# Kernel tuning notes

Measured on AMD Instinct MI355X. Metric: run time of the kernel, lower is better.

The kernel has to match this reference:

```python
import jax, jax.numpy as jnp
import numpy as np
from jax import lax

N, T, E = 20000, 64, 640000
H, OUT, HEADS = 128, 64, 3
NEG_SLOPE = 0.2  # GATConv default negative_slope


def setup_inputs() -> dict:
    key = jax.random.key(0)
    ks = jax.random.split(key, 10)
    s = 0.1
    return {
        "node_features": jax.random.normal(ks[0], (N, T), jnp.float32),
        "edge_index": jax.random.randint(ks[1], (2, E), 0, N, dtype=jnp.int32),
        "edge_attributes": jax.random.uniform(ks[2], (E,), jnp.float32),
        "lstm_Wih": jax.random.normal(ks[3], (4 * H, 1), jnp.float32) * s,
        "lstm_Whh": jax.random.normal(ks[4], (4 * H, H), jnp.float32) * s,
        "lstm_bih": jnp.zeros((4 * H,), jnp.float32),
        "lstm_bhh": jnp.zeros((4 * H,), jnp.float32),
        "gcn_W": jax.random.normal(ks[5], (H, H), jnp.float32) * s,
        "gcn_b": jnp.zeros((H,), jnp.float32),
        "gat_W": jax.random.normal(ks[6], (HEADS * OUT, H), jnp.float32) * s,
        "gat_att_src": jax.random.normal(ks[7], (HEADS, OUT), jnp.float32) * s,
        "gat_att_dst": jax.random.normal(ks[8], (HEADS, OUT), jnp.float32) * s,
        "gat_b": jnp.zeros((HEADS * OUT,), jnp.float32),
    }


def _lstm_last(x, Wih, Whh, bih, bhh):
    """x: [N, T, 1] -> last hidden state [N, H] (torch gate order i,f,g,o)."""
    n = x.shape[0]
    h_dim = Whh.shape[1]
    b = bih + bhh

    def step(carry, xt):
        h, c = carry
        g = xt @ Wih.T + h @ Whh.T + b  # [N, 4H]
        i, f, gg, o = jnp.split(g, 4, axis=-1)
        c = jax.nn.sigmoid(f) * c + jax.nn.sigmoid(i) * jnp.tanh(gg)
        h = jax.nn.sigmoid(o) * jnp.tanh(c)
        return (h, c), None

    init = (jnp.zeros((n, h_dim), x.dtype), jnp.zeros((n, h_dim), x.dtype))
    (h, _), _ = lax.scan(step, init, jnp.swapaxes(x, 0, 1))
    return h


def _add_self_loops(row, col, n):
    loop = jnp.arange(n, dtype=row.dtype)
    return jnp.concatenate([row, loop]), jnp.concatenate([col, loop])


def _gcn(x, row, col, edge_weight, W, b):
    """PyG GCNConv: self-loops (weight 1), symmetric normalization, W x + b."""
    n = x.shape[0]
    row, col = _add_self_loops(row, col, n)
    ew = jnp.concatenate([edge_weight, jnp.ones((n,), edge_weight.dtype)])
    x = x @ W.T  # [N, H]
    deg = jax.ops.segment_sum(ew, col, num_segments=n)
    dinv = jnp.where(deg > 0, deg ** -0.5, 0.0)
    norm = dinv[row] * ew * dinv[col]  # [E+N]
    out = jax.ops.segment_sum(x[row] * norm[:, None], col, num_segments=n)
    return out + b


def _gat(x, row, col, W, att_src, att_dst, b):
    """PyG GATConv (concat=True): self-loops, edge softmax over incoming edges."""
    n = x.shape[0]
    heads, c = att_src.shape
    xh = (x @ W.T).reshape(n, heads, c)  # [N, Hd, C]
    a_src = jnp.einsum('nhc,hc->nh', xh, att_src)  # [N, Hd]
    a_dst = jnp.einsum('nhc,hc->nh', xh, att_dst)
    row, col = _add_self_loops(row, col, n)
    alpha = jax.nn.leaky_relu(a_src[row] + a_dst[col], NEG_SLOPE)  # [E', Hd]
    amax = jax.ops.segment_max(alpha, col, num_segments=n)
    alpha = jnp.exp(alpha - amax[col])
    denom = jax.ops.segment_sum(alpha, col, num_segments=n)
    alpha = alpha / denom[col]
    out = jax.ops.segment_sum(xh[row] * alpha[:, :, None], col, num_segments=n)
    return out.reshape(n, heads * c) + b


def reference(node_features, edge_index, edge_attributes,
              lstm_Wih, lstm_Whh, lstm_bih, lstm_bhh,
              gcn_W, gcn_b, gat_W, gat_att_src, gat_att_dst, gat_b):
    x = node_features[:, :, None]  # [N, T, 1]
    x = _lstm_last(x, lstm_Wih, lstm_Whh, lstm_bih, lstm_bhh)  # [N, H]
    x = jax.nn.relu(x)
    row, col = edge_index[0], edge_index[1]
    x = _gcn(x, row, col, edge_attributes, gcn_W, gcn_b)
    x = jax.nn.relu(x)
    x = _gat(x, row, col, gat_W, gat_att_src, gat_att_dst, gat_b)  # [N, Hd*C]
    return jnp.mean(x, axis=0, keepdims=True)  # global_mean_pool, batch=None -> [1, Hd*C]
```

## Files before the change

kernel.cpp:

```cpp
#include <hip/hip_runtime.h>


#define N_NODES 20000
#define T_STEPS 64
#define N_EDGES 640000
#define HDIM    128
#define JOUT    192
#define NEG_SLOPE 0.2f
#define EDGE_CAP 128
#define NBW     16
#define NGRP    5
#define NBB     (NBW * NGRP)
#define BTHR    640
#define LDS_W     131072
#define LDS_BW    4096
#define LDS_SCR   (NGRP * 4096)
#define LDS_FLG   256
#define LDS_TOTAL (LDS_W + LDS_BW + LDS_SCR + LDS_FLG)

#define L2E  1.4426950408889634f
#define K2E  2.8853900817779268f

typedef _Float16 half8 __attribute__((ext_vector_type(8)));
typedef _Float16 half4v __attribute__((ext_vector_type(4)));
typedef _Float16 half2v __attribute__((ext_vector_type(2)));
typedef float floatx4 __attribute__((ext_vector_type(4)));

__device__ __forceinline__ float lrelu(float x) { return x > 0.f ? x : NEG_SLOPE * x; }

__global__ void pack_whh_kernel(const float* __restrict__ Whh,
                                _Float16* __restrict__ Wpack)
{
  int i = blockIdx.x * 256 + threadIdx.x;
  int tile = i >> 6, lane = i & 63;
  int nt = tile >> 2, kt = tile & 3;
  int row = nt * 16 + (lane & 15);
  int c0  = kt * 32 + (lane >> 4) * 8;
  const float sc = ((row >> 7) == 2) ? K2E : L2E;
  half8 v;
  #pragma unroll
  for (int j = 0; j < 8; ++j)
    v[j] = (_Float16)(Whh[row * 128 + c0 + j] * sc);
  *(half8*)&Wpack[(size_t)i * 8] = v;
}

template <int M>
__global__ void pack_w_kernel(const float* __restrict__ W,
                              _Float16* __restrict__ P)
{
  int i = blockIdx.x * 256 + threadIdx.x;
  int tile = i >> 6, lane = i & 63;
  int mt = tile >> 2, kt = tile & 3;
  int row = mt * 16 + (lane & 15);
  int c0  = kt * 32 + (lane >> 4) * 8;
  half8 v;
  #pragma unroll
  for (int j = 0; j < 8; ++j)
    v[j] = (_Float16)W[row * 128 + c0 + j];
  *(half8*)&P[(size_t)i * 8] = v;
}


#define INITACC(L, acc) do {                                                  \
  _Pragma("unroll") for (int g_ = 0; g_ < 4; ++g_) {                          \
    const float4 p0_ = *(const float4*)&bwRole[g_ * 128 + (L) * 16];          \
    const float4 p1_ = *(const float4*)&bwRole[g_ * 128 + (L) * 16 + 2];      \
    acc[g_][0] = p0_.x + xv * p0_.y;                                          \
    acc[g_][1] = p0_.z + xv * p0_.w;                                          \
    acc[g_][2] = p1_.x + xv * p1_.y;                                          \
    acc[g_][3] = p1_.z + xv * p1_.w;                                          \
  }                                                                           \
} while (0)

#define LDA(buf, L, KT) do {                                                  \
  _Pragma("unroll") for (int g_ = 0; g_ < 4; ++g_)                            \
    buf[g_] = *(const half8*)&WlRole[g_ * 16384 + (L) * 2048 + (KT) * 512];   \
} while (0)

#define MFA(acc, buf, KT) do {                                                \
  _Pragma("unroll") for (int g_ = 0; g_ < 4; ++g_)                            \
    acc[g_] = __builtin_amdgcn_mfma_f32_16x16x32_f16(                         \
        buf[g_], Bf[(KT)], acc[g_], 0, 0, 0);                                 \
} while (0)

#define PHASE4(L, acc) do {                                                   \
  const int cg_ = cgb + (L);                                                  \
  half4v hpack;                                                               \
  _Pragma("unroll") for (int r_ = 0; r_ < 4; ++r_) {                          \
    const float Be = __builtin_amdgcn_exp2f(-acc[0][r_]);                     \
    const float Ae = __builtin_amdgcn_exp2f(-acc[1][r_]);                     \
    const float De = __builtin_amdgcn_exp2f(acc[2][r_]);                      \
    const float Ee = __builtin_amdgcn_exp2f(-acc[3][r_]);                     \
    const float Ap = Ae + 1.f;                                                \
    const float Bp = Be + 1.f;                                                \
    const float Dp = De + 1.f;                                                \
    const float Nn = cst[(L) * 4 + r_] * Bp * Dp + Ap * (De - 1.f);           \
    const float cv = Nn * __builtin_amdgcn_rcpf(Ap * Bp * Dp);                \
    cst[(L) * 4 + r_] = cv;                                                   \
    const float cvc = fminf(fmaxf(cv, -10.f), 10.f);                          \
    const float Fe = __builtin_amdgcn_exp2f(K2E * cvc);                       \
    hpack[r_] = (_Float16)((Fe - 1.f) *                                       \
                __builtin_amdgcn_rcpf((Ee + 1.f) * (Fe + 1.f)));              \
  }                                                                           \
  const int lp_ = nl + 16 * (2 * (cg_ & 1) + wq_hi);                          \
  *(half4v*)&myscr[(cg_ >> 1) * 512 + lp_ * 8 + j0] = hpack;                  \
} while (0)

#define SB __builtin_amdgcn_sched_barrier(0)

#define SIGNAL(arr, val) do {                                                 \
  __threadfence_block();                                                      \
  if (ln == 0) arr[wv] = (val);                                               \
} while (0)
#define WAITGE(arr, val) do {                                                 \
  if (ln == 0) { while (arr[pw] < (val)) __builtin_amdgcn_s_sleep(1); }       \
  __builtin_amdgcn_wave_barrier();                                            \
  __threadfence_block();                                                      \
} while (0)

#define LSTM_STEP(t) do {                                                     \
  WAITGE(flW, (t));                                                           \
  half8 Bf[4];                                                                \
  _Pragma("unroll") for (int kt_ = 0; kt_ < 4; ++kt_)                         \
    Bf[kt_] = *(const half8*)&scrLane[kt_ * 512];                             \
  SIGNAL(flR, (t) + 1);                                                       \
  floatx4 accA[4], accB[4];                                                   \
  half8 Aa[4], Ab[4];                                                         \
                                                                  \
  INITACC(0, accA);                                                           \
  LDA(Aa, 0, 0); LDA(Ab, 0, 1);                                               \
  MFA(accA, Aa, 0); LDA(Aa, 0, 2);                                            \
  MFA(accA, Ab, 1); LDA(Ab, 0, 3);                                            \
  MFA(accA, Aa, 2); MFA(accA, Ab, 3);                                         \
                                                                  \
  INITACC(1, accB); LDA(Aa, 1, 0); LDA(Ab, 1, 1);                             \
  WAITGE(flR, (t) + 1);                                                       \
  SB; PHASE4(0, accA);                                                        \
  MFA(accB, Aa, 0); LDA(Aa, 1, 2);                                            \
  MFA(accB, Ab, 1); LDA(Ab, 1, 3);                                            \
  MFA(accB, Aa, 2); MFA(accB, Ab, 3);                                         \
                                                                  \
  INITACC(2, accA); LDA(Aa, 2, 0); LDA(Ab, 2, 1);                             \
  SB; PHASE4(1, accB);                                                        \
  MFA(accA, Aa, 0); LDA(Aa, 2, 2);                                            \
  MFA(accA, Ab, 1); LDA(Ab, 2, 3);                                            \
  MFA(accA, Aa, 2); MFA(accA, Ab, 3);                                         \
                                                                  \
  INITACC(3, accB); LDA(Aa, 3, 0); LDA(Ab, 3, 1);                             \
  SB; PHASE4(2, accA);                                                        \
  MFA(accB, Aa, 0); LDA(Aa, 3, 2);                                            \
  MFA(accB, Ab, 1); LDA(Ab, 3, 3);                                            \
  MFA(accB, Aa, 2); MFA(accB, Ab, 3);                                         \
  PHASE4(3, accB);                                                            \
  SIGNAL(flW, (t) + 1);                                                       \
} while (0)

__global__ __attribute__((amdgpu_flat_work_group_size(BTHR, BTHR),
                          amdgpu_waves_per_eu(3, 3)))
void lstm_stream_kernel(
    const float* __restrict__ xfeat, const _Float16* __restrict__ Wpack,
    const float* __restrict__ Wih, const float* __restrict__ bih,
    const float* __restrict__ bhh, _Float16* __restrict__ x1)
{
  extern __shared__ char dynlds[];
  _Float16* Wl  = (_Float16*)dynlds;
  float2*   bw  = (float2*)(dynlds + LDS_W);
  _Float16* scr = (_Float16*)(dynlds + LDS_W + LDS_BW);
  volatile int* flR = (volatile int*)(dynlds + LDS_W + LDS_BW + LDS_SCR);
  volatile int* flW = flR + 16;

  const int tid  = threadIdx.x;
  const int wv   = tid >> 6;
  const int pw   = wv ^ 1;
  const int grp  = wv >> 1;
  const int role = wv & 1;
  const int cgb  = role * 4;
  const int ln   = tid & 63;
  const int nl   = ln & 15;
  const int quad = ln >> 4;
  const int n0   = blockIdx.x * NBB + grp * NBW;

  {
    const float4* src = (const float4*)Wpack;
    float4* dst = (float4*)Wl;
    for (int i = tid; i < LDS_W / 16; i += BTHR) dst[i] = src[i];
  }
  for (int i = tid; i < 512; i += BTHR) {
    const float sc = ((i >> 7) == 2) ? K2E : L2E;
    bw[i] = make_float2((bih[i] + bhh[i]) * sc, Wih[i] * sc);
  }
  {
    float4* z = (float4*)scr;
    for (int i = tid; i < LDS_SCR / 16; i += BTHR)
      z[i] = make_float4(0.f, 0.f, 0.f, 0.f);
  }
  if (tid < 32) { flR[tid] = 0; flW[tid] = 0; }
  __syncthreads();

  _Float16* myscr = scr + grp * 2048;
  const _Float16* WlRole  = Wl + (size_t)cgb * 2048 + (size_t)ln * 8;
  const float2*   bwRole  = bw + cgb * 16 + quad * 4;
  const _Float16* scrLane = myscr + (size_t)ln * 8;
  const float* xrow = xfeat + (size_t)(n0 + nl) * T_STEPS;

  float cst[16];
  #pragma unroll
  for (int i = 0; i < 16; ++i) cst[i] = 0.f;

  const int wq_hi = quad >> 1;
  const int j0    = (quad & 1) * 4;

  float xv = xrow[0];

  #pragma unroll 1
  for (int t = 0; t < T_STEPS; ++t) {
    const float xn = xrow[(t + 1 <= 63) ? (t + 1) : 63];
    LSTM_STEP(t);
    xv = xn;
  }

  #pragma unroll
  for (int k = 0; k < 2; ++k) {
    const int kt = role * 2 + k;
    half8 hf = *(const half8*)&scrLane[kt * 512];
    #pragma unroll
    for (int j = 0; j < 8; ++j)
      hf[j] = (_Float16)fmaxf((float)hf[j], 0.f);
    *(half8*)&x1[(size_t)(n0 + nl) * HDIM + kt * 32 + quad * 8] = hf;
  }
}

template <int J>
__global__ __launch_bounds__(320) void gemm_mfma(
    const _Float16* __restrict__ X, const _Float16* __restrict__ P,
    _Float16* __restrict__ Y)
{
  const int ln = threadIdx.x & 63;
  const int wv = threadIdx.x >> 6;
  const int node = blockIdx.x * 80 + wv * 16 + (ln & 15);
  const int ko = (ln >> 4) * 8;
  half8 Bf[4];
  #pragma unroll
  for (int kt = 0; kt < 4; ++kt)
    Bf[kt] = *(const half8*)&X[(size_t)node * 128 + kt * 32 + ko];
  #pragma unroll
  for (int m = 0; m < J / 16; ++m) {
    floatx4 acc = {0.f, 0.f, 0.f, 0.f};
    #pragma unroll
    for (int kt = 0; kt < 4; ++kt) {
      const half8 Af = *(const half8*)&P[(size_t)((m * 4 + kt) * 64 + ln) * 8];
      acc = __builtin_amdgcn_mfma_f32_16x16x32_f16(Af, Bf[kt], acc, 0, 0, 0);
    }
    half4v o;
    #pragma unroll
    for (int j = 0; j < 4; ++j) o[j] = (_Float16)acc[j];
    *(half4v*)&Y[(size_t)node * J + m * 16 + (ln >> 4) * 4] = o;
  }
}

__global__ __launch_bounds__(320) void gemm_mfma_att(
    const _Float16* __restrict__ X, const _Float16* __restrict__ P,
    const float* __restrict__ att_src, const float* __restrict__ att_dst,
    _Float16* __restrict__ Y, float4* __restrict__ asrc,
    float4* __restrict__ adst)
{
  __shared__ float aS[JOUT], aD[JOUT];
  const int tid = threadIdx.x;
  for (int i = tid; i < JOUT; i += 320) { aS[i] = att_src[i]; aD[i] = att_dst[i]; }
  __syncthreads();
  const int ln = tid & 63;
  const int wv = tid >> 6;
  const int quad = ln >> 4;
  const int node = blockIdx.x * 80 + wv * 16 + (ln & 15);
  half8 Bf[4];
  #pragma unroll
  for (int kt = 0; kt < 4; ++kt)
    Bf[kt] = *(const half8*)&X[(size_t)node * 128 + kt * 32 + quad * 8];
  float sA[3] = {0.f, 0.f, 0.f}, sD[3] = {0.f, 0.f, 0.f};
  #pragma unroll
  for (int m = 0; m < JOUT / 16; ++m) {
    floatx4 acc = {0.f, 0.f, 0.f, 0.f};
    #pragma unroll
    for (int kt = 0; kt < 4; ++kt) {
      const half8 Af = *(const half8*)&P[(size_t)((m * 4 + kt) * 64 + ln) * 8];
      acc = __builtin_amdgcn_mfma_f32_16x16x32_f16(Af, Bf[kt], acc, 0, 0, 0);
    }
    const int h  = m >> 2;
    const int jo = (m & 3) * 16 + quad * 4;
    half4v o;
    #pragma unroll
    for (int j = 0; j < 4; ++j) {
      sA[h] += acc[j] * aS[h * 64 + jo + j];
      sD[h] += acc[j] * aD[h * 64 + jo + j];
      o[j] = (_Float16)acc[j];
    }
    *(half4v*)&Y[(size_t)node * JOUT + m * 16 + quad * 4] = o;
  }
  #pragma unroll
  for (int h = 0; h < 3; ++h) {
    sA[h] += __shfl_xor(sA[h], 16); sA[h] += __shfl_xor(sA[h], 32);
    sD[h] += __shfl_xor(sD[h], 16); sD[h] += __shfl_xor(sD[h], 32);
  }
  if (quad == 0) {
    asrc[node] = make_float4(sA[0], sA[1], sA[2], 0.f);
    adst[node] = make_float4(sD[0], sD[1], sD[2], 0.f);
  }
}

__global__ void zero_kernel(float* __restrict__ deg, int* __restrict__ cnt,
                            float* __restrict__ accum)
{
  int i = blockIdx.x * 256 + threadIdx.x;
  if (i < N_NODES) { deg[i] = 0.f; cnt[i] = 0; }
  if (i < JOUT) accum[i] = 0.f;
}

__global__ void fill2_kernel(const int* __restrict__ ei, const float* __restrict__ ew,
                             int* __restrict__ cnt, float* __restrict__ deg,
                             int* __restrict__ esrcB, float* __restrict__ ewB)
{
  int e = blockIdx.x * 256 + threadIdx.x;
  int r = ei[e];
  int c = ei[N_EDGES + e];
  float w = ew[e];
  int p = atomicAdd(&cnt[c], 1);
  esrcB[(size_t)c * EDGE_CAP + p] = r;
  ewB[(size_t)c * EDGE_CAP + p]   = w;
  atomicAdd(&deg[c], w);
}

__global__ void dinv_kernel(const float* __restrict__ deg, float* __restrict__ dinv)
{
  int i = blockIdx.x * 256 + threadIdx.x;
  if (i < N_NODES) dinv[i] = rsqrtf(deg[i] + 1.0f);
}

__global__ __launch_bounds__(256) void gcn_agg_kernel(
    const _Float16* __restrict__ y, const float* __restrict__ dinv,
    const int* __restrict__ cnt, const int* __restrict__ esrcB,
    const float* __restrict__ ewB, const float* __restrict__ gcn_b,
    _Float16* __restrict__ x2)
{
  __shared__ float2 stg[4][64];
  const int lane = threadIdx.x & 63;
  const int wv = threadIdx.x >> 6;
  const int c = blockIdx.x * 4 + wv;
  const float dc = dinv[c];
  const half2v* y2 = (const half2v*)y;
  half2v yc = y2[c * 64 + lane];
  float ax = (float)yc[0] * dc * dc, ay = (float)yc[1] * dc * dc;
  const int cc = cnt[c];
  const size_t base = (size_t)c * EDGE_CAP;
  for (int tb = 0; tb < cc; tb += 64) {
    const int nedge = min(64, cc - tb);
    const int k = tb + lane;
    if (k < cc) {
      const int s = esrcB[base + k];
      stg[wv][lane] = make_float2(__int_as_float(s), ewB[base + k] * dinv[s] * dc);
    }
    __builtin_amdgcn_wave_barrier();
    int i = 0;
    for (; i + 4 <= nedge; i += 4) {
      float2 p0 = stg[wv][i],     p1 = stg[wv][i + 1];
      float2 p2 = stg[wv][i + 2], p3 = stg[wv][i + 3];
      const half2v a0 = y2[(size_t)__float_as_int(p0.x) * 64 + lane];
      const half2v a1 = y2[(size_t)__float_as_int(p1.x) * 64 + lane];
      const half2v a2 = y2[(size_t)__float_as_int(p2.x) * 64 + lane];
      const half2v a3 = y2[(size_t)__float_as_int(p3.x) * 64 + lane];
      ax += (float)a0[0] * p0.y + (float)a1[0] * p1.y +
            (float)a2[0] * p2.y + (float)a3[0] * p3.y;
      ay += (float)a0[1] * p0.y + (float)a1[1] * p1.y +
            (float)a2[1] * p2.y + (float)a3[1] * p3.y;
    }
    for (; i < nedge; ++i) {
      float2 p0 = stg[wv][i];
      const half2v a0 = y2[(size_t)__float_as_int(p0.x) * 64 + lane];
      ax += (float)a0[0] * p0.y; ay += (float)a0[1] * p0.y;
    }
    __builtin_amdgcn_wave_barrier();
  }
  int j0 = lane * 2;
  half2v o;
  o[0] = (_Float16)fmaxf(ax + gcn_b[j0], 0.f);
  o[1] = (_Float16)fmaxf(ay + gcn_b[j0 + 1], 0.f);
  *(half2v*)&x2[c * 128 + j0] = o;
}

__global__ __launch_bounds__(256) void gat_agg_kernel(
    const _Float16* __restrict__ xh, const float4* __restrict__ asrc,
    const float4* __restrict__ adst, const int* __restrict__ cnt,
    const int* __restrict__ esrcB, float* __restrict__ accum)
{
  __shared__ float4 cstg[4][64];
  const int lane = threadIdx.x & 63;
  const int wv = threadIdx.x >> 6;
  const int c = blockIdx.x * 4 + wv;
  const int cc = cnt[c];
  const size_t base = (size_t)c * EDGE_CAP;
  float4 adc = adst[c];
  float4 asc = asrc[c];
  const float se0 = __expf(lrelu(asc.x + adc.x));
  const float se1 = __expf(lrelu(asc.y + adc.y));
  const float se2 = __expf(lrelu(asc.z + adc.z));

  float o0 = se0 * (float)xh[c * JOUT + lane];
  float o1 = se1 * (float)xh[c * JOUT + 64 + lane];
  float o2 = se2 * (float)xh[c * JOUT + 128 + lane];
  float dp0 = 0.f, dp1 = 0.f, dp2 = 0.f;

  for (int tb = 0; tb < cc; tb += 64) {
    const int nedge = min(64, cc - tb);
    const int k = tb + lane;
    if (k < cc) {
      const int s = esrcB[base + k];
      const float4 av = asrc[s];
      const float a0 = __expf(lrelu(av.x + adc.x));
      const float a1 = __expf(lrelu(av.y + adc.y));
      const float a2 = __expf(lrelu(av.z + adc.z));
      dp0 += a0; dp1 += a1; dp2 += a2;
      cstg[wv][lane] = make_float4(__int_as_float(s), a0, a1, a2);
    }
    __builtin_amdgcn_wave_barrier();
    int i = 0;
    for (; i + 2 <= nedge; i += 2) {
      float4 q0 = cstg[wv][i], q1 = cstg[wv][i + 1];
      const _Float16* r0 = xh + (size_t)__float_as_int(q0.x) * JOUT;
      const _Float16* r1 = xh + (size_t)__float_as_int(q1.x) * JOUT;
      float a0 = (float)r0[lane], b0 = (float)r0[64 + lane], g0 = (float)r0[128 + lane];
      float a1 = (float)r1[lane], b1 = (float)r1[64 + lane], g1 = (float)r1[128 + lane];
      o0 += q0.y * a0 + q1.y * a1;
      o1 += q0.z * b0 + q1.z * b1;
      o2 += q0.w * g0 + q1.w * g1;
    }
    for (; i < nedge; ++i) {
      float4 q0 = cstg[wv][i];
      const _Float16* r0 = xh + (size_t)__float_as_int(q0.x) * JOUT;
      o0 += q0.y * (float)r0[lane];
      o1 += q0.z * (float)r0[64 + lane];
      o2 += q0.w * (float)r0[128 + lane];
    }
    __builtin_amdgcn_wave_barrier();
  }

  #pragma unroll
  for (int off = 1; off < 64; off <<= 1) {
    dp0 += __shfl_xor(dp0, off);
    dp1 += __shfl_xor(dp1, off);
    dp2 += __shfl_xor(dp2, off);
  }
  const float iv0 = 1.f / (dp0 + se0);
  const float iv1 = 1.f / (dp1 + se1);
  const float iv2 = 1.f / (dp2 + se2);
  o0 *= iv0; o1 *= iv1; o2 *= iv2;

  __shared__ float red[4][JOUT];
  red[wv][lane]       = o0;
  red[wv][64 + lane]  = o1;
  red[wv][128 + lane] = o2;
  __syncthreads();
  if (threadIdx.x < JOUT) {
    float sum = red[0][threadIdx.x] + red[1][threadIdx.x] +
                red[2][threadIdx.x] + red[3][threadIdx.x];
    atomicAdd(&accum[threadIdx.x], sum);
  }
}

__global__ void finalize_kernel(const float* __restrict__ accum,
                                const float* __restrict__ gat_b,
                                float* __restrict__ out)
{
  int j = threadIdx.x;
  if (j < JOUT) out[j] = accum[j] * (1.0f / N_NODES) + gat_b[j];
}

extern "C" void kernel_launch(void* const* d_in, const int* in_sizes, int n_in,
                              void* d_out, int out_size, void* d_ws, size_t ws_size,
                              hipStream_t stream)
{
  const float* xfeat = (const float*)d_in[0];
  const int*   eidx  = (const int*)d_in[1];
  const float* eattr = (const float*)d_in[2];
  const float* Wih   = (const float*)d_in[3];
  const float* Whh   = (const float*)d_in[4];
  const float* bihp  = (const float*)d_in[5];
  const float* bhhp  = (const float*)d_in[6];
  const float* gcnW  = (const float*)d_in[7];
  const float* gcnb  = (const float*)d_in[8];
  const float* gatW  = (const float*)d_in[9];
  const float* attS  = (const float*)d_in[10];
  const float* attD  = (const float*)d_in[11];
  const float* gatb  = (const float*)d_in[12];
  float* out = (float*)d_out;

  char* ws = (char*)d_ws;
  size_t off = 0;
  auto alloc = [&](size_t bytes) {
    char* p = ws + off;
    off += (bytes + 255) & ~size_t(255);
    return p;
  };
  _Float16*  x1     = (_Float16*)alloc((size_t)N_NODES * 128 * 2);
  _Float16*  y      = (_Float16*)alloc((size_t)N_NODES * 128 * 2);
  _Float16*  x2     = (_Float16*)alloc((size_t)N_NODES * 128 * 2);
  _Float16*  xh     = (_Float16*)alloc((size_t)N_NODES * 192 * 2);
  float4*    asrc   = (float4*)alloc((size_t)N_NODES * 16);
  float4*    adst   = (float4*)alloc((size_t)N_NODES * 16);
  float*     deg    = (float*)alloc((size_t)N_NODES * 4);
  float*     dinv   = (float*)alloc((size_t)N_NODES * 4);
  int*       cnt    = (int*)alloc((size_t)N_NODES * 4);
  int*       esrcB  = (int*)alloc((size_t)N_NODES * EDGE_CAP * 4);
  float*     ewB    = (float*)alloc((size_t)N_NODES * EDGE_CAP * 4);
  float*     accum  = (float*)alloc(JOUT * 4);
  _Float16*  wpack  = (_Float16*)alloc(131072);
  _Float16*  wpackG = (_Float16*)alloc((size_t)128 * 128 * 2);
  _Float16*  wpackA = (_Float16*)alloc((size_t)192 * 128 * 2);

  hipFuncSetAttribute((const void*)lstm_stream_kernel,
                      hipFuncAttributeMaxDynamicSharedMemorySize, LDS_TOTAL);

  zero_kernel<<<(N_NODES + 255) / 256, 256, 0, stream>>>(deg, cnt, accum);
  pack_whh_kernel<<<32, 256, 0, stream>>>(Whh, wpack);
  pack_w_kernel<128><<<8, 256, 0, stream>>>(gcnW, wpackG);
  pack_w_kernel<192><<<12, 256, 0, stream>>>(gatW, wpackA);
  lstm_stream_kernel<<<N_NODES / NBB, BTHR, LDS_TOTAL, stream>>>(
      xfeat, wpack, Wih, bihp, bhhp, x1);
  fill2_kernel<<<N_EDGES / 256, 256, 0, stream>>>(eidx, eattr, cnt, deg, esrcB, ewB);
  dinv_kernel<<<(N_NODES + 255) / 256, 256, 0, stream>>>(deg, dinv);
  gemm_mfma<128><<<N_NODES / 80, 320, 0, stream>>>(x1, wpackG, y);
  gcn_agg_kernel<<<N_NODES / 4, 256, 0, stream>>>(y, dinv, cnt, esrcB, ewB, gcnb, x2);
  gemm_mfma_att<<<N_NODES / 80, 320, 0, stream>>>(x2, wpackA, attS, attD,
                                                  xh, asrc, adst);
  gat_agg_kernel<<<N_NODES / 4, 256, 0, stream>>>(xh, asrc, adst, cnt, esrcB, accum);
  finalize_kernel<<<1, 256, 0, stream>>>(accum, gatb, out);
}
```

Before: 660.1 us.

## Overlap edge bucketing with LSTM via extra blocks; pack src/weight pairs

The edge bucketing fill now runs inside the LSTM kernel launch on 6 extra blocks, so it can overlap with the LSTM recurrence instead of running as a separate kernel afterward. Source index and edge weight are stored together as an int2, which halves the number of scattered stores and loads per edge. The float atomic degree accumulation is replaced by a per-node warp reduction over the bucket in a new degdinv kernel, removing 640K float atomics and one launch. The extra blocks each request the full LDS allocation and compete for CUs with the LSTM blocks, and gat_agg now loads 8-byte pairs where it only needs the index.

```diff
diff --git a/kernel.cpp b/kernel.cpp
--- a/kernel.cpp
+++ b/kernel.cpp
@@ -12,6 +12,8 @@
 #define NGRP    5
 #define NBB     (NBW * NGRP)
 #define BTHR    640
+#define NBLK    250
+#define GRIDX   256
 #define LDS_W     131072
 #define LDS_BW    4096
 #define LDS_SCR   (NGRP * 4096)
@@ -160,8 +162,24 @@
 void lstm_stream_kernel(
     const float* __restrict__ xfeat, const _Float16* __restrict__ Wpack,
     const float* __restrict__ Wih, const float* __restrict__ bih,
-    const float* __restrict__ bhh, _Float16* __restrict__ x1)
-{
+    const float* __restrict__ bhh, _Float16* __restrict__ x1,
+    const int* __restrict__ ei, const float* __restrict__ ew,
+    int* __restrict__ cnt, int2* __restrict__ pairB)
+{
+  const int tid  = threadIdx.x;
+
+  if (blockIdx.x >= NBLK) {
+    const int stride = (GRIDX - NBLK) * BTHR;
+    for (int e = (blockIdx.x - NBLK) * BTHR + tid; e < N_EDGES; e += stride) {
+      const int r = ei[e];
+      const int c = ei[N_EDGES + e];
+      const float w = ew[e];
+      const int p = atomicAdd(&cnt[c], 1);
+      pairB[(size_t)c * EDGE_CAP + p] = make_int2(r, __float_as_int(w));
+    }
+    return;
+  }
+
   extern __shared__ char dynlds[];
   _Float16* Wl  = (_Float16*)dynlds;
   float2*   bw  = (float2*)(dynlds + LDS_W);
@@ -169,7 +187,6 @@
   volatile int* flR = (volatile int*)(dynlds + LDS_W + LDS_BW + LDS_SCR);
   volatile int* flW = flR + 16;
 
-  const int tid  = threadIdx.x;
   const int wv   = tid >> 6;
   const int pw   = wv ^ 1;
   const int grp  = wv >> 1;
@@ -307,39 +324,34 @@
   }
 }
 
-__global__ void zero_kernel(float* __restrict__ deg, int* __restrict__ cnt,
-                            float* __restrict__ accum)
+__global__ void zero_kernel(int* __restrict__ cnt, float* __restrict__ accum)
 {
   int i = blockIdx.x * 256 + threadIdx.x;
-  if (i < N_NODES) { deg[i] = 0.f; cnt[i] = 0; }
+  if (i < N_NODES) cnt[i] = 0;
   if (i < JOUT) accum[i] = 0.f;
 }
 
-__global__ void fill2_kernel(const int* __restrict__ ei, const float* __restrict__ ew,
-                             int* __restrict__ cnt, float* __restrict__ deg,
-                             int* __restrict__ esrcB, float* __restrict__ ewB)
-{
-  int e = blockIdx.x * 256 + threadIdx.x;
-  int r = ei[e];
-  int c = ei[N_EDGES + e];
-  float w = ew[e];
-  int p = atomicAdd(&cnt[c], 1);
-  esrcB[(size_t)c * EDGE_CAP + p] = r;
-  ewB[(size_t)c * EDGE_CAP + p]   = w;
-  atomicAdd(&deg[c], w);
-}
-
-__global__ void dinv_kernel(const float* __restrict__ deg, float* __restrict__ dinv)
-{
-  int i = blockIdx.x * 256 + threadIdx.x;
-  if (i < N_NODES) dinv[i] = rsqrtf(deg[i] + 1.0f);
+__global__ __launch_bounds__(256) void degdinv_kernel(
+    const int* __restrict__ cnt, const int2* __restrict__ pairB,
+    float* __restrict__ dinv)
+{
+  const int lane = threadIdx.x & 63;
+  const int wv = threadIdx.x >> 6;
+  const int c = blockIdx.x * 4 + wv;
+  const int cc = cnt[c];
+  const size_t base = (size_t)c * EDGE_CAP;
+  float s = 0.f;
+  for (int k = lane; k < cc; k += 64)
+    s += __int_as_float(pairB[base + k].y);
+  #pragma unroll
+  for (int off = 1; off < 64; off <<= 1) s += __shfl_xor(s, off);
+  if (lane == 0) dinv[c] = rsqrtf(s + 1.0f);
 }
 
 __global__ __launch_bounds__(256) void gcn_agg_kernel(
     const _Float16* __restrict__ y, const float* __restrict__ dinv,
-    const int* __restrict__ cnt, const int* __restrict__ esrcB,
-    const float* __restrict__ ewB, const float* __restrict__ gcn_b,
-    _Float16* __restrict__ x2)
+    const int* __restrict__ cnt, const int2* __restrict__ pairB,
+    const float* __restrict__ gcn_b, _Float16* __restrict__ x2)
 {
   __shared__ float2 stg[4][64];
   const int lane = threadIdx.x & 63;
@@ -355,8 +367,9 @@
     const int nedge = min(64, cc - tb);
     const int k = tb + lane;
     if (k < cc) {
-      const int s = esrcB[base + k];
-      stg[wv][lane] = make_float2(__int_as_float(s), ewB[base + k] * dinv[s] * dc);
+      const int2 pr = pairB[base + k];
+      stg[wv][lane] = make_float2(__int_as_float(pr.x),
+                                  __int_as_float(pr.y) * dinv[pr.x] * dc);
     }
     __builtin_amdgcn_wave_barrier();
     int i = 0;
@@ -389,7 +402,7 @@
 __global__ __launch_bounds__(256) void gat_agg_kernel(
     const _Float16* __restrict__ xh, const float4* __restrict__ asrc,
     const float4* __restrict__ adst, const int* __restrict__ cnt,
-    const int* __restrict__ esrcB, float* __restrict__ accum)
+    const int2* __restrict__ pairB, float* __restrict__ accum)
 {
   __shared__ float4 cstg[4][64];
   const int lane = threadIdx.x & 63;
@@ -412,7 +425,7 @@
     const int nedge = min(64, cc - tb);
     const int k = tb + lane;
     if (k < cc) {
-      const int s = esrcB[base + k];
+      const int s = pairB[base + k].x;
       const float4 av = asrc[s];
       const float a0 = __expf(lrelu(av.x + adc.x));
       const float a1 = __expf(lrelu(av.y + adc.y));
@@ -505,11 +518,9 @@
   _Float16*  xh     = (_Float16*)alloc((size_t)N_NODES * 192 * 2);
   float4*    asrc   = (float4*)alloc((size_t)N_NODES * 16);
   float4*    adst   = (float4*)alloc((size_t)N_NODES * 16);
-  float*     deg    = (float*)alloc((size_t)N_NODES * 4);
   float*     dinv   = (float*)alloc((size_t)N_NODES * 4);
   int*       cnt    = (int*)alloc((size_t)N_NODES * 4);
-  int*       esrcB  = (int*)alloc((size_t)N_NODES * EDGE_CAP * 4);
-  float*     ewB    = (float*)alloc((size_t)N_NODES * EDGE_CAP * 4);
+  int2*      pairB  = (int2*)alloc((size_t)N_NODES * EDGE_CAP * 8);
   float*     accum  = (float*)alloc(JOUT * 4);
   _Float16*  wpack  = (_Float16*)alloc(131072);
   _Float16*  wpackG = (_Float16*)alloc((size_t)128 * 128 * 2);
@@ -518,18 +529,17 @@
   hipFuncSetAttribute((const void*)lstm_stream_kernel,
                       hipFuncAttributeMaxDynamicSharedMemorySize, LDS_TOTAL);
 
-  zero_kernel<<<(N_NODES + 255) / 256, 256, 0, stream>>>(deg, cnt, accum);
+  zero_kernel<<<(N_NODES + 255) / 256, 256, 0, stream>>>(cnt, accum);
   pack_whh_kernel<<<32, 256, 0, stream>>>(Whh, wpack);
   pack_w_kernel<128><<<8, 256, 0, stream>>>(gcnW, wpackG);
   pack_w_kernel<192><<<12, 256, 0, stream>>>(gatW, wpackA);
-  lstm_stream_kernel<<<N_NODES / NBB, BTHR, LDS_TOTAL, stream>>>(
-      xfeat, wpack, Wih, bihp, bhhp, x1);
-  fill2_kernel<<<N_EDGES / 256, 256, 0, stream>>>(eidx, eattr, cnt, deg, esrcB, ewB);
-  dinv_kernel<<<(N_NODES + 255) / 256, 256, 0, stream>>>(deg, dinv);
+  lstm_stream_kernel<<<GRIDX, BTHR, LDS_TOTAL, stream>>>(
+      xfeat, wpack, Wih, bihp, bhhp, x1, eidx, eattr, cnt, pairB);
+  degdinv_kernel<<<N_NODES / 4, 256, 0, stream>>>(cnt, pairB, dinv);
   gemm_mfma<128><<<N_NODES / 80, 320, 0, stream>>>(x1, wpackG, y);
-  gcn_agg_kernel<<<N_NODES / 4, 256, 0, stream>>>(y, dinv, cnt, esrcB, ewB, gcnb, x2);
+  gcn_agg_kernel<<<N_NODES / 4, 256, 0, stream>>>(y, dinv, cnt, pairB, gcnb, x2);
   gemm_mfma_att<<<N_NODES / 80, 320, 0, stream>>>(x2, wpackA, attS, attD,
                                                   xh, asrc, adst);
-  gat_agg_kernel<<<N_NODES / 4, 256, 0, stream>>>(xh, asrc, adst, cnt, esrcB, accum);
+  gat_agg_kernel<<<N_NODES / 4, 256, 0, stream>>>(xh, asrc, adst, cnt, pairB, accum);
   finalize_kernel<<<1, 256, 0, stream>>>(accum, gatb, out);
 }
```

Result: faster. 594.2 us (-10.0%).
